# Performance work log

Measured on AMD Instinct MI355X. Metric: run time of the kernel, lower is better.

Reference implementation:

```python
import jax, jax.numpy as jnp
import numpy as np

IN_F, OUT_F, LAT, RES, K, B = 512, 512, 512, 64, 3, 8
EPS = 1e-08
C_LIN = 1.0 / np.sqrt(LAT)          # EqualizedWeight scale for linear
C_CONV = 1.0 / np.sqrt(IN_F * K * K)  # EqualizedWeight scale for conv


def setup_inputs() -> dict:
    key = jax.random.key(0)
    k1, k2, k3, k4 = jax.random.split(key, 4)
    return {
        "x": jax.random.normal(k1, (B, IN_F, RES, RES), dtype=jnp.float32),
        "latent": jax.random.normal(k2, (B, LAT), dtype=jnp.float32),
        "w_lin": jax.random.normal(k3, (IN_F, LAT), dtype=jnp.float32),
        "b_lin": jnp.ones((IN_F,), dtype=jnp.float32),
        "w_conv": jax.random.normal(k4, (OUT_F, IN_F, K, K), dtype=jnp.float32),
        "b_conv": jnp.zeros((OUT_F,), dtype=jnp.float32),
    }


def reference(x, latent, w_lin, b_lin, w_conv, b_conv):
    # EqualizedLinear: s = latent @ (w_lin*c).T + b_lin*lr_mul  -> [B, IN_F]
    s = latent @ (w_lin * C_LIN).T + b_lin
    # ModulatedConv2d. Per-sample weight w[b,o,i,k,k] = (w_conv*c)[o,i,k,k]*s[b,i],
    # demodulated by sigma_inv[b,o] = rsqrt(sum_{i,k,k} w^2 + eps).
    w = w_conv * C_CONV  # [O, I, K, K]
    # sum_{k,k} w^2 over spatial -> [O, I], then contract with s^2 -> [B, O]
    w2 = jnp.sum(w * w, axis=(2, 3))  # [O, I]
    sigma_inv = jax.lax.rsqrt(jnp.einsum('oi,bi->bo', w2, s * s) + EPS)
    # conv(x, w*s_b) == conv(x * s_b, w): modulate input, single batched conv,
    # then demodulate output per (b, o). Avoids materializing B*O filters.
    x_mod = x * s[:, :, None, None]
    y = jax.lax.conv_general_dilated(
        x_mod, w,
        window_strides=(1, 1),
        padding=[((K - 1) // 2, (K - 1) // 2)] * 2,
        dimension_numbers=('NCHW', 'OIHW', 'NCHW'),
    )
    y = y * sigma_inv[:, :, None, None] + b_conv[None, :, None, None]
    return y
```

## Files before the change

### kernel.cpp

```cpp
#include <hip/hip_runtime.h>
#include <hip/hip_bf16.h>

#define IN_F 512
#define OUT_F 512
#define LATD 512
#define RES 64
#define BATCH 8
#define EPSV 1e-8f

static constexpr float C_LIN  = 0.04419417382415922f;
static constexpr float C_CONV = 0.014731391274719739f;

typedef __attribute__((ext_vector_type(8))) short short8;
typedef __attribute__((ext_vector_type(4))) float f32x4;

union BF { __hip_bfloat16 h; short s; };

__device__ __forceinline__ void async_load16(const char* g, char* l) {
  __builtin_amdgcn_global_load_lds(
      (const __attribute__((address_space(1))) unsigned int*)g,
      (__attribute__((address_space(3))) unsigned int*)l, 16, 0, 0);
}

__global__ void k_compute_s(const float* __restrict__ latent,
                            const float* __restrict__ w_lin,
                            const float* __restrict__ b_lin,
                            float* __restrict__ s) {
  const int i = blockIdx.x;
  const int lane = threadIdx.x;
  float acc[BATCH];
#pragma unroll
  for (int b = 0; b < BATCH; ++b) acc[b] = 0.f;
  for (int l = lane; l < LATD; l += 64) {
    const float wv = w_lin[i * LATD + l];
#pragma unroll
    for (int b = 0; b < BATCH; ++b) acc[b] += wv * latent[b * LATD + l];
  }
#pragma unroll
  for (int b = 0; b < BATCH; ++b) {
    float v = acc[b];
#pragma unroll
    for (int off = 32; off > 0; off >>= 1) v += __shfl_down(v, off);
    if (lane == 0) s[b * IN_F + i] = v * C_LIN + b_lin[i];
  }
}

__global__ void k_prep_w(const float* __restrict__ w_conv,
                         short* __restrict__ wb) {
  const int t = blockIdx.x * 256 + threadIdx.x;
  const int part = t & 3;
  const int u = t >> 2;
  const int o = u & 511;
  const int v = u >> 9;
  const int ic = v / 9;
  const int tap = v - ic * 9;
  short8 pk;
#pragma unroll
  for (int j = 0; j < 8; ++j) {
    const int i = ic * 32 + part * 8 + j;
    BF cv; cv.h = __float2bfloat16(w_conv[((size_t)o * IN_F + i) * 9 + tap] * C_CONV);
    pk[j] = cv.s;
  }
  *(short8*)(wb + (((size_t)(ic * 9 + tap) * OUT_F + o) * 32 + part * 8)) = pk;
}

__global__ void k_sigma(const float* __restrict__ w_conv,
                        const float* __restrict__ s,
                        float* __restrict__ sigma_inv) {
  const int o = blockIdx.x;
  const int lane = threadIdx.x;
  float acc[BATCH];
#pragma unroll
  for (int b = 0; b < BATCH; ++b) acc[b] = 0.f;
  for (int i = lane; i < IN_F; i += 64) {
    const float* wp = w_conv + (size_t)(o * IN_F + i) * 9;
    float w2 = 0.f;
#pragma unroll
    for (int t = 0; t < 9; ++t) { const float w = wp[t] * C_CONV; w2 += w * w; }
#pragma unroll
    for (int b = 0; b < BATCH; ++b) {
      const float sv = s[b * IN_F + i];
      acc[b] += w2 * sv * sv;
    }
  }
#pragma unroll
  for (int b = 0; b < BATCH; ++b) {
    float v = acc[b];
#pragma unroll
    for (int off = 32; off > 0; off >>= 1) v += __shfl_down(v, off);
    if (lane == 0) sigma_inv[b * OUT_F + o] = rsqrtf(v + EPSV);
  }
}

__global__ void k_zero_border(char* __restrict__ xmp) {
  const int plane = blockIdx.x;
  char* base = xmp + (size_t)plane * (66 * 66 * 64);
  for (int idx = threadIdx.x; idx < 1040; idx += 256) {
    const int c = idx >> 2, part = idx & 3;
    int hp, wp;
    if (c < 66)       { hp = 0;          wp = c; }
    else if (c < 132) { hp = 65;         wp = c - 66; }
    else if (c < 196) { hp = c - 132 + 1; wp = 0; }
    else              { hp = c - 196 + 1; wp = 65; }
    *(uint4*)(base + ((size_t)hp * 66 + wp) * 64 + part * 16) = make_uint4(0u, 0u, 0u, 0u);
  }
}

__global__ void k_modulate(const float* __restrict__ x,
                           const float* __restrict__ s,
                           char* __restrict__ xmp) {
  const int h  = blockIdx.x & 63;
  const int ic = (blockIdx.x >> 6) & 15;
  const int b  = blockIdx.x >> 10;
  __shared__ float tile[32][65];
  const int tid = threadIdx.x;
  {
    const int il = tid >> 3, w8 = (tid & 7) * 8;
    const int i = ic * 32 + il;
    const float sv = s[b * IN_F + i];
    const float* xp = x + (((size_t)(b * IN_F + i) * RES + h) * RES + w8);
    const float4 v0 = *(const float4*)xp;
    const float4 v1 = *(const float4*)(xp + 4);
    tile[il][w8 + 0] = v0.x * sv; tile[il][w8 + 1] = v0.y * sv;
    tile[il][w8 + 2] = v0.z * sv; tile[il][w8 + 3] = v0.w * sv;
    tile[il][w8 + 4] = v1.x * sv; tile[il][w8 + 5] = v1.y * sv;
    tile[il][w8 + 6] = v1.z * sv; tile[il][w8 + 7] = v1.w * sv;
  }
  __syncthreads();
  {
    const int w = tid >> 2, part = tid & 3;
    short8 pk;
#pragma unroll
    for (int j = 0; j < 8; ++j) {
      BF cv; cv.h = __float2bfloat16(tile[part * 8 + j][w]);
      pk[j] = cv.s;
    }
    char* dst = xmp + ((size_t)((ic * 8 + b) * 66 + (h + 1)) * 66 + (w + 1)) * 64 + part * 16;
    *(short8*)dst = pk;
  }
}

__global__ __launch_bounds__(256, 2)
void k_conv(const char* __restrict__ xmp,
            const short* __restrict__ wb,
            const float* __restrict__ sigma_inv,
            const float* __restrict__ b_conv,
            float* __restrict__ out) {
  __shared__ __align__(16) char lds[57344];
  char* const wsm = lds + 45056;
  const int o0 = blockIdx.x * 64;
  const int b  = blockIdx.y >> 3;
  const int h0 = (blockIdx.y & 7) * 8;
  const int tid = threadIdx.x;
  const int wave = tid >> 6, lane = tid & 63;
  const int lo = lane & 15, quad = lane >> 4;
  const int qb = quad * 16;

  f32x4 acc[8][4];
#pragma unroll
  for (int i = 0; i < 8; ++i)
#pragma unroll
    for (int j = 0; j < 4; ++j) acc[i][j] = (f32x4){0.f, 0.f, 0.f, 0.f};

  for (int ic = 0; ic < 16; ++ic) {
    const char* xr = xmp + (size_t)((ic * 8 + b) * 66 + h0) * (66 * 64);
    const char* wr = (const char*)(wb + (size_t)(ic * 9) * OUT_F * 32) + (size_t)o0 * 64;
#pragma unroll 1
    for (int dh = 0; dh < 3; ++dh) {
      __syncthreads();
      if (dh == 0) {
#pragma unroll
        for (int k = 0; k < 11; ++k) {
          const int j = tid + k * 256;
          const int jj = j > 2639 ? 2639 : j;
          const int p = jj >> 2;
          const int q = (jj & 3) ^ ((p >> 1) & 3);
          async_load16(xr + p * 64 + q * 16, lds + j * 16);
        }
      }
#pragma unroll
      for (int k = 0; k < 3; ++k) {
        const int j = k * 256 + tid;
        const int cell = j >> 2;
        const int q = (j & 3) ^ ((cell >> 1) & 3);
        const int ol = cell & 63;
        async_load16(wr + (size_t)((dh * 3 + k) * OUT_F + ol) * 64 + q * 16, wsm + j * 16);
      }
      __syncthreads();
#pragma unroll
      for (int dw = 0; dw < 3; ++dw) {
        const int cb = dw * 64 + lo;
        const int baddr = ((cb << 6) | qb) ^ ((cb << 3) & 0x30);
        short8 bf[4];
#pragma unroll
        for (int ns = 0; ns < 4; ++ns)
          bf[ns] = *(const short8*)(wsm + baddr + ns * 1024);
#pragma unroll
        for (int row = 0; row < 2; ++row) {
          const int p0 = (wave * 2 + row + dh) * 66 + dw + lo;
          const int aaddr = ((p0 << 6) | qb) ^ ((p0 << 3) & 0x30);
#pragma unroll
          for (int seg = 0; seg < 4; ++seg) {
            const short8 af = *(const short8*)(lds + aaddr + seg * 1024);
#pragma unroll
            for (int ns = 0; ns < 4; ++ns)
              acc[row * 4 + seg][ns] =
                  __builtin_amdgcn_mfma_f32_16x16x32_bf16(af, bf[ns], acc[row * 4 + seg][ns], 0, 0, 0);
          }
        }
      }
    }
  }
#pragma unroll
  for (int ns = 0; ns < 4; ++ns) {
    const int o = o0 + ns * 16 + lo;
    const float sig  = sigma_inv[b * OUT_F + o];
    const float bias = b_conv[o];
#pragma unroll
    for (int row = 0; row < 2; ++row) {
      float* op = out + ((size_t)(b * OUT_F + o) * RES + (h0 + wave * 2 + row)) * RES;
#pragma unroll
      for (int seg = 0; seg < 4; ++seg) {
        f32x4 v;
#pragma unroll
        for (int r = 0; r < 4; ++r) v[r] = acc[row * 4 + seg][ns][r] * sig + bias;
        *(f32x4*)(op + seg * 16 + quad * 4) = v;
      }
    }
  }
}

extern "C" void kernel_launch(void* const* d_in, const int* in_sizes, int n_in,
                              void* d_out, int out_size, void* d_ws, size_t ws_size,
                              hipStream_t stream) {
  const float* x      = (const float*)d_in[0];
  const float* latent = (const float*)d_in[1];
  const float* w_lin  = (const float*)d_in[2];
  const float* b_lin  = (const float*)d_in[3];
  const float* w_conv = (const float*)d_in[4];
  const float* b_conv = (const float*)d_in[5];
  float* out = (float*)d_out;

  char* ws = (char*)d_ws;
  char*  xmp       = ws;
  short* wb        = (short*)(ws + 35684352);
  float* s         = (float*)(ws + 40402944);
  float* sigma_inv = (float*)(ws + 40419328);

  k_compute_s<<<IN_F, 64, 0, stream>>>(latent, w_lin, b_lin, s);
  k_prep_w<<<1152, 256, 0, stream>>>(w_conv, wb);
  k_sigma<<<OUT_F, 64, 0, stream>>>(w_conv, s, sigma_inv);
  k_zero_border<<<128, 256, 0, stream>>>(xmp);
  k_modulate<<<BATCH * 16 * RES, 256, 0, stream>>>(x, s, xmp);
  dim3 grid(OUT_F / 64, BATCH * 8);
  k_conv<<<grid, 256, 0, stream>>>(xmp, wb, sigma_inv, b_conv, out);
}
```

Measured before the change: 273.6 us.

## Rework conv kernel with 32x32 MFMA, 16-channel chunks, and double-buffered LDS

The implicit-GEMM conv kernel is restructured to use 32x32x16 bf16 MFMA, 16-channel input chunks with a new padded input layout and weight layout, and double-buffered async global-to-LDS loads that prefetch the next chunk while computing the current one. The earlier per-dh staging and its extra barriers go away. The kernel now has one barrier per chunk and overlaps memory with MFMA work. Prep kernels are also changed: the weight-prep kernel emits per-(o,i) squared sums so sigma no longer rereads w_conv, and compute_s uses vectorised loads. Risks include the larger LDS footprint (79 KB) limiting occupancy, unswizzled LDS reads causing bank conflicts, and scalar uncoalesced output stores in the epilogue.

```diff
diff --git a/kernel.cpp b/kernel.cpp
--- a/kernel.cpp
+++ b/kernel.cpp
@@ -11,8 +11,8 @@
 static constexpr float C_LIN  = 0.04419417382415922f;
 static constexpr float C_CONV = 0.014731391274719739f;
 
-typedef __attribute__((ext_vector_type(8))) short short8;
-typedef __attribute__((ext_vector_type(4))) float f32x4;
+typedef __attribute__((ext_vector_type(8)))  short short8;
+typedef __attribute__((ext_vector_type(16))) float f32x16;
 
 union BF { __hip_bfloat16 h; short s; };
 
@@ -28,13 +28,15 @@
                             float* __restrict__ s) {
   const int i = blockIdx.x;
   const int lane = threadIdx.x;
+  const float4* wl = (const float4*)(w_lin + (size_t)i * LATD);
+  const float4 w0 = wl[lane * 2], w1 = wl[lane * 2 + 1];
   float acc[BATCH];
 #pragma unroll
-  for (int b = 0; b < BATCH; ++b) acc[b] = 0.f;
-  for (int l = lane; l < LATD; l += 64) {
-    const float wv = w_lin[i * LATD + l];
-#pragma unroll
-    for (int b = 0; b < BATCH; ++b) acc[b] += wv * latent[b * LATD + l];
+  for (int b = 0; b < BATCH; ++b) {
+    const float4* lt = (const float4*)(latent + (size_t)b * LATD);
+    const float4 l0 = lt[lane * 2], l1 = lt[lane * 2 + 1];
+    acc[b] = w0.x * l0.x + w0.y * l0.y + w0.z * l0.z + w0.w * l0.w +
+             w1.x * l1.x + w1.y * l1.y + w1.z * l1.z + w1.w * l1.w;
   }
 #pragma unroll
   for (int b = 0; b < BATCH; ++b) {
@@ -46,41 +48,40 @@
 }
 
 __global__ void k_prep_w(const float* __restrict__ w_conv,
-                         short* __restrict__ wb) {
+                         short* __restrict__ wb,
+                         float* __restrict__ w2) {
   const int t = blockIdx.x * 256 + threadIdx.x;
-  const int part = t & 3;
-  const int u = t >> 2;
-  const int o = u & 511;
-  const int v = u >> 9;
-  const int ic = v / 9;
-  const int tap = v - ic * 9;
-  short8 pk;
-#pragma unroll
-  for (int j = 0; j < 8; ++j) {
-    const int i = ic * 32 + part * 8 + j;
-    BF cv; cv.h = __float2bfloat16(w_conv[((size_t)o * IN_F + i) * 9 + tap] * C_CONV);
-    pk[j] = cv.s;
-  }
-  *(short8*)(wb + (((size_t)(ic * 9 + tap) * OUT_F + o) * 32 + part * 8)) = pk;
-}
-
-__global__ void k_sigma(const float* __restrict__ w_conv,
+  const int o = t >> 9;
+  const int i = t & 511;
+  const float* src = w_conv + (size_t)t * 9;
+  const int c = i >> 4, ob = o >> 6, ol = o & 63, i16 = i & 15;
+  float sum = 0.f;
+#pragma unroll
+  for (int tap = 0; tap < 9; ++tap) {
+    const float v = src[tap] * C_CONV;
+    sum += v * v;
+    BF cv; cv.h = __float2bfloat16(v);
+    wb[(size_t)((c * 8 + ob) * 9 + tap) * 1024 + ol * 16 + i16] = cv.s;
+  }
+  w2[t] = sum;
+}
+
+__global__ void k_sigma(const float* __restrict__ w2,
                         const float* __restrict__ s,
                         float* __restrict__ sigma_inv) {
-  const int o = blockIdx.x;
-  const int lane = threadIdx.x;
+  const int o = blockIdx.x * 4 + (threadIdx.x >> 6);
+  const int lane = threadIdx.x & 63;
   float acc[BATCH];
 #pragma unroll
   for (int b = 0; b < BATCH; ++b) acc[b] = 0.f;
-  for (int i = lane; i < IN_F; i += 64) {
-    const float* wp = w_conv + (size_t)(o * IN_F + i) * 9;
-    float w2 = 0.f;
-#pragma unroll
-    for (int t = 0; t < 9; ++t) { const float w = wp[t] * C_CONV; w2 += w * w; }
+#pragma unroll
+  for (int k = 0; k < 8; ++k) {
+    const int i = k * 64 + lane;
+    const float w = w2[o * IN_F + i];
 #pragma unroll
     for (int b = 0; b < BATCH; ++b) {
       const float sv = s[b * IN_F + i];
-      acc[b] += w2 * sv * sv;
+      acc[b] += w * sv * sv;
     }
   }
 #pragma unroll
@@ -93,30 +94,29 @@
 }
 
 __global__ void k_zero_border(char* __restrict__ xmp) {
-  const int plane = blockIdx.x;
-  char* base = xmp + (size_t)plane * (66 * 66 * 64);
-  for (int idx = threadIdx.x; idx < 1040; idx += 256) {
-    const int c = idx >> 2, part = idx & 3;
+  char* base = xmp + (size_t)blockIdx.x * 139392;
+  for (int q = threadIdx.x; q < 520; q += 256) {
+    const int cell = q >> 1, half = q & 1;
     int hp, wp;
-    if (c < 66)       { hp = 0;          wp = c; }
-    else if (c < 132) { hp = 65;         wp = c - 66; }
-    else if (c < 196) { hp = c - 132 + 1; wp = 0; }
-    else              { hp = c - 196 + 1; wp = 65; }
-    *(uint4*)(base + ((size_t)hp * 66 + wp) * 64 + part * 16) = make_uint4(0u, 0u, 0u, 0u);
+    if (cell < 66)       { hp = 0;              wp = cell; }
+    else if (cell < 132) { hp = 65;             wp = cell - 66; }
+    else if (cell < 196) { hp = cell - 132 + 1; wp = 0; }
+    else                 { hp = cell - 196 + 1; wp = 65; }
+    *(uint4*)(base + ((size_t)hp * 66 + wp) * 32 + half * 16) = make_uint4(0u, 0u, 0u, 0u);
   }
 }
 
 __global__ void k_modulate(const float* __restrict__ x,
                            const float* __restrict__ s,
                            char* __restrict__ xmp) {
-  const int h  = blockIdx.x & 63;
-  const int ic = (blockIdx.x >> 6) & 15;
-  const int b  = blockIdx.x >> 10;
+  const int h    = blockIdx.x & 63;
+  const int ic32 = (blockIdx.x >> 6) & 15;
+  const int b    = blockIdx.x >> 10;
   __shared__ float tile[32][65];
   const int tid = threadIdx.x;
   {
     const int il = tid >> 3, w8 = (tid & 7) * 8;
-    const int i = ic * 32 + il;
+    const int i = ic32 * 32 + il;
     const float sv = s[b * IN_F + i];
     const float* xp = x + (((size_t)(b * IN_F + i) * RES + h) * RES + w8);
     const float4 v0 = *(const float4*)xp;
@@ -129,102 +129,116 @@
   __syncthreads();
   {
     const int w = tid >> 2, part = tid & 3;
+    const int chalf = part >> 1, half = part & 1;
     short8 pk;
 #pragma unroll
     for (int j = 0; j < 8; ++j) {
-      BF cv; cv.h = __float2bfloat16(tile[part * 8 + j][w]);
+      BF cv; cv.h = __float2bfloat16(tile[chalf * 16 + half * 8 + j][w]);
       pk[j] = cv.s;
     }
-    char* dst = xmp + ((size_t)((ic * 8 + b) * 66 + (h + 1)) * 66 + (w + 1)) * 64 + part * 16;
+    const int c = ic32 * 2 + chalf;
+    char* dst = xmp + (size_t)(c * 8 + b) * 139392 +
+                ((size_t)(h + 1) * 66 + (w + 1)) * 32 + half * 16;
     *(short8*)dst = pk;
   }
 }
 
 __global__ __launch_bounds__(256, 2)
 void k_conv(const char* __restrict__ xmp,
-            const short* __restrict__ wb,
+            const short* __restrict__ wbg,
             const float* __restrict__ sigma_inv,
             const float* __restrict__ b_conv,
             float* __restrict__ out) {
-  __shared__ __align__(16) char lds[57344];
-  char* const wsm = lds + 45056;
-  const int o0 = blockIdx.x * 64;
+  __shared__ __align__(16) char lds[79104];
+  const int ob = blockIdx.x;
+  const int o0 = ob * 64;
   const int b  = blockIdx.y >> 3;
   const int h0 = (blockIdx.y & 7) * 8;
   const int tid = threadIdx.x;
   const int wave = tid >> 6, lane = tid & 63;
-  const int lo = lane & 15, quad = lane >> 4;
-  const int qb = quad * 16;
-
-  f32x4 acc[8][4];
-#pragma unroll
-  for (int i = 0; i < 8; ++i)
-#pragma unroll
-    for (int j = 0; j < 4; ++j) acc[i][j] = (f32x4){0.f, 0.f, 0.f, 0.f};
-
-  for (int ic = 0; ic < 16; ++ic) {
-    const char* xr = xmp + (size_t)((ic * 8 + b) * 66 + h0) * (66 * 64);
-    const char* wr = (const char*)(wb + (size_t)(ic * 9) * OUT_F * 32) + (size_t)o0 * 64;
-#pragma unroll 1
-    for (int dh = 0; dh < 3; ++dh) {
-      __syncthreads();
-      if (dh == 0) {
-#pragma unroll
-        for (int k = 0; k < 11; ++k) {
-          const int j = tid + k * 256;
-          const int jj = j > 2639 ? 2639 : j;
-          const int p = jj >> 2;
-          const int q = (jj & 3) ^ ((p >> 1) & 3);
-          async_load16(xr + p * 64 + q * 16, lds + j * 16);
+  const int l31 = lane & 31, half = lane >> 5;
+
+  f32x16 acc[2][4];
+#pragma unroll
+  for (int i = 0; i < 2; ++i)
+#pragma unroll
+    for (int j = 0; j < 4; ++j)
+#pragma unroll
+      for (int r = 0; r < 16; ++r) acc[i][j][r] = 0.f;
+
+  const char* xsrc0 = xmp + (size_t)b * 139392 + (size_t)h0 * 2112;
+  const char* wsrc0 = (const char*)wbg + (size_t)ob * 18432;
+
+#pragma unroll
+  for (int k = 0; k < 5; ++k) {
+    const int j = tid + k * 256;
+    async_load16(xsrc0 + j * 16, lds + j * 16);
+  }
+  if (tid < 40) { const int j = 1280 + tid; async_load16(xsrc0 + j * 16, lds + j * 16); }
+#pragma unroll
+  for (int k = 0; k < 4; ++k) {
+    const int j = tid + k * 256;
+    async_load16(wsrc0 + j * 16, lds + 42240 + j * 16);
+  }
+  if (tid < 128) { const int j = 1024 + tid; async_load16(wsrc0 + j * 16, lds + 42240 + j * 16); }
+  __syncthreads();
+
+  for (int ic = 0; ic < 32; ++ic) {
+    const int p = ic & 1;
+    if (ic + 1 < 32) {
+      const char* xs = xsrc0 + (size_t)(ic + 1) * (8 * 139392);
+      const char* wsr = wsrc0 + (size_t)(ic + 1) * (8 * 18432);
+      char* xd = lds + (p ^ 1) * 21120;
+      char* wd = lds + 42240 + (p ^ 1) * 18432;
+#pragma unroll
+      for (int k = 0; k < 5; ++k) {
+        const int j = tid + k * 256;
+        async_load16(xs + j * 16, xd + j * 16);
+      }
+      if (tid < 40) { const int j = 1280 + tid; async_load16(xs + j * 16, xd + j * 16); }
+#pragma unroll
+      for (int k = 0; k < 4; ++k) {
+        const int j = tid + k * 256;
+        async_load16(wsr + j * 16, wd + j * 16);
+      }
+      if (tid < 128) { const int j = 1024 + tid; async_load16(wsr + j * 16, wd + j * 16); }
+    }
+    const char* xp = lds + p * 21120;
+    const char* wp = lds + 42240 + p * 18432;
+#pragma unroll
+    for (int tap = 0; tap < 9; ++tap) {
+      const int dh = tap / 3, dw = tap - dh * 3;
+      const short8 a0 = *(const short8*)(wp + (tap * 64 + l31) * 32 + half * 16);
+      const short8 a1 = *(const short8*)(wp + (tap * 64 + 32 + l31) * 32 + half * 16);
+#pragma unroll
+      for (int tp = 0; tp < 4; ++tp) {
+        const int hr = wave * 2 + (tp >> 1) + dh;
+        const int wc = (tp & 1) * 32 + dw + l31;
+        const short8 bf = *(const short8*)(xp + (hr * 66 + wc) * 32 + half * 16);
+        acc[0][tp] = __builtin_amdgcn_mfma_f32_32x32x16_bf16(a0, bf, acc[0][tp], 0, 0, 0);
+        acc[1][tp] = __builtin_amdgcn_mfma_f32_32x32x16_bf16(a1, bf, acc[1][tp], 0, 0, 0);
+      }
+    }
+    __syncthreads();
+  }
+
+#pragma unroll
+  for (int t_o = 0; t_o < 2; ++t_o) {
+#pragma unroll
+    for (int g = 0; g < 4; ++g) {
+#pragma unroll
+      for (int r = 0; r < 4; ++r) {
+        const int o = o0 + t_o * 32 + r + 8 * g + 4 * half;
+        const float sig  = sigma_inv[b * OUT_F + o];
+        const float bias = b_conv[o];
+        const int reg = g * 4 + r;
+#pragma unroll
+        for (int tp = 0; tp < 4; ++tp) {
+          const int h = h0 + wave * 2 + (tp >> 1);
+          const int w = (tp & 1) * 32 + l31;
+          out[(((size_t)(b * OUT_F + o) * RES + h) * RES) + w] =
+              acc[t_o][tp][reg] * sig + bias;
         }
-      }
-#pragma unroll
-      for (int k = 0; k < 3; ++k) {
-        const int j = k * 256 + tid;
-        const int cell = j >> 2;
-        const int q = (j & 3) ^ ((cell >> 1) & 3);
-        const int ol = cell & 63;
-        async_load16(wr + (size_t)((dh * 3 + k) * OUT_F + ol) * 64 + q * 16, wsm + j * 16);
-      }
-      __syncthreads();
-#pragma unroll
-      for (int dw = 0; dw < 3; ++dw) {
-        const int cb = dw * 64 + lo;
-        const int baddr = ((cb << 6) | qb) ^ ((cb << 3) & 0x30);
-        short8 bf[4];
-#pragma unroll
-        for (int ns = 0; ns < 4; ++ns)
-          bf[ns] = *(const short8*)(wsm + baddr + ns * 1024);
-#pragma unroll
-        for (int row = 0; row < 2; ++row) {
-          const int p0 = (wave * 2 + row + dh) * 66 + dw + lo;
-          const int aaddr = ((p0 << 6) | qb) ^ ((p0 << 3) & 0x30);
-#pragma unroll
-          for (int seg = 0; seg < 4; ++seg) {
-            const short8 af = *(const short8*)(lds + aaddr + seg * 1024);
-#pragma unroll
-            for (int ns = 0; ns < 4; ++ns)
-              acc[row * 4 + seg][ns] =
-                  __builtin_amdgcn_mfma_f32_16x16x32_bf16(af, bf[ns], acc[row * 4 + seg][ns], 0, 0, 0);
-          }
-        }
-      }
-    }
-  }
-#pragma unroll
-  for (int ns = 0; ns < 4; ++ns) {
-    const int o = o0 + ns * 16 + lo;
-    const float sig  = sigma_inv[b * OUT_F + o];
-    const float bias = b_conv[o];
-#pragma unroll
-    for (int row = 0; row < 2; ++row) {
-      float* op = out + ((size_t)(b * OUT_F + o) * RES + (h0 + wave * 2 + row)) * RES;
-#pragma unroll
-      for (int seg = 0; seg < 4; ++seg) {
-        f32x4 v;
-#pragma unroll
-        for (int r = 0; r < 4; ++r) v[r] = acc[row * 4 + seg][ns][r] * sig + bias;
-        *(f32x4*)(op + seg * 16 + quad * 4) = v;
       }
     }
   }
@@ -244,13 +258,14 @@
   char* ws = (char*)d_ws;
   char*  xmp       = ws;
   short* wb        = (short*)(ws + 35684352);
-  float* s         = (float*)(ws + 40402944);
-  float* sigma_inv = (float*)(ws + 40419328);
+  float* w2        = (float*)(ws + 40402944);
+  float* s         = (float*)(ws + 41451520);
+  float* sigma_inv = (float*)(ws + 41467904);
 
   k_compute_s<<<IN_F, 64, 0, stream>>>(latent, w_lin, b_lin, s);
-  k_prep_w<<<1152, 256, 0, stream>>>(w_conv, wb);
-  k_sigma<<<OUT_F, 64, 0, stream>>>(w_conv, s, sigma_inv);
-  k_zero_border<<<128, 256, 0, stream>>>(xmp);
+  k_prep_w<<<1024, 256, 0, stream>>>(w_conv, wb, w2);
+  k_sigma<<<128, 256, 0, stream>>>(w2, s, sigma_inv);
+  k_zero_border<<<256, 256, 0, stream>>>(xmp);
   k_modulate<<<BATCH * 16 * RES, 256, 0, stream>>>(x, s, xmp);
   dim3 grid(OUT_F / 64, BATCH * 8);
   k_conv<<<grid, 256, 0, stream>>>(xmp, wb, sigma_inv, b_conv, out);
```

After: 253.0 us. 7.5% less time.
